# Kernel tuning notes

Measured on AMD Instinct MI355X. Metric: run time of the kernel, lower is better.

The kernel has to match this reference:

```python
import jax, jax.numpy as jnp
import numpy as np

T = 2048        # num tokens
HID = 2048      # hidden_size
HQ = 16         # num_heads
HKV = 8         # num_kv_heads
D = 128         # head_dim
P = 2           # power retention exponent
THETA = 10000.0 # rope base
SCALE = D ** -0.5


def setup_inputs() -> dict:
    key = jax.random.key(0)
    ks = jax.random.split(key, 8)
    s = 0.02
    return {
        "positions": jnp.arange(T, dtype=jnp.int64) if jax.config.jax_enable_x64 else jnp.arange(T, dtype=jnp.int32),
        "hidden_states": jax.random.normal(ks[0], (T, HID), jnp.float32),
        "Wq": jax.random.normal(ks[1], (HID, HQ * D), jnp.float32) * s,
        "bq": jnp.zeros((HQ * D,), jnp.float32),
        "Wk": jax.random.normal(ks[2], (HID, HKV * D), jnp.float32) * s,
        "bk": jnp.zeros((HKV * D,), jnp.float32),
        "Wv": jax.random.normal(ks[3], (HID, HKV * D), jnp.float32) * s,
        "bv": jnp.zeros((HKV * D,), jnp.float32),
        "Wg": jax.random.normal(ks[4], (HID, HKV), jnp.float32) * s,
        "bg": jnp.zeros((HKV,), jnp.float32),
        "Wo": jax.random.normal(ks[5], (HQ * D, HID), jnp.float32) * s,
        "bo": jnp.zeros((HID,), jnp.float32),
    }


def _rope_neox(x, pos):
    # x: [T, H, D], pos: [T]; rotate-half (neox) style, rotary_dim == head_dim
    half = D // 2
    inv_freq = 1.0 / (THETA ** (jnp.arange(0, D, 2, dtype=jnp.float32) / D))  # [D/2]
    freqs = pos.astype(jnp.float32)[:, None] * inv_freq                        # [T, D/2]
    cos = jnp.cos(freqs)[:, None, :]
    sin = jnp.sin(freqs)[:, None, :]
    x1, x2 = x[..., :half], x[..., half:]
    return jnp.concatenate([x1 * cos - x2 * sin, x2 * cos + x1 * sin], axis=-1)


def reference(positions, hidden_states, Wq, bq, Wk, bk, Wv, bv, Wg, bg, Wo, bo):
    # QKVG projections
    q = (hidden_states @ Wq + bq).reshape(T, HQ, D)
    k = (hidden_states @ Wk + bk).reshape(T, HKV, D)
    v = (hidden_states @ Wv + bv).reshape(T, HKV, D)
    g = hidden_states @ Wg + bg            # [T, HKV], one gate scalar per kv head

    # RoPE on q/k, logsigmoid gate in fp32
    q = _rope_neox(q, positions)
    k = _rope_neox(k, positions)
    g = jax.nn.log_sigmoid(g.astype(jnp.float32))   # [T, HKV], <= 0
    G = jnp.cumsum(g, axis=0)                       # [T, HKV] cumulative log-decay

    # GQA: expand kv heads to query heads
    rep = HQ // HKV
    k = jnp.repeat(k, rep, axis=1)   # [T, HQ, D]
    v = jnp.repeat(v, rep, axis=1)
    G = jnp.repeat(G, rep, axis=1)   # [T, HQ]

    # Power retention (quadratic attention form, seq_len <= switch_over_seq_len):
    # W_ij = (scale * q_i . k_j)^p * exp(G_i - G_j), causal j <= i
    S = jnp.einsum('thd,shd->hts', q, k) * SCALE      # [H, T, T]
    S = S ** P
    Gh = G.T                                          # [H, T]
    mask = jnp.tril(jnp.ones((T, T), dtype=bool))
    diff = jnp.where(mask[None], Gh[:, :, None] - Gh[:, None, :], -jnp.inf)
    W = S * jnp.exp(diff)                             # decay<=1 inside mask, 0 outside

    out = jnp.einsum('hts,shd->thd', W, v)            # [T, H, D]
    out = out.reshape(T, HQ * D) @ Wo + bo            # o_proj
    return out
```

## Files before the change

kernel.cpp:

```cpp
#include <hip/hip_runtime.h>
#include <hip/hip_bf16.h>
#include <math.h>

#define T_SEQ 2048
#define HID 2048
#define HQ 16
#define HKV 8
#define D_HEAD 128
#define HALF 64
#define SCALE_F 0.08838834764831845f
#define PROJW 4096

typedef __attribute__((ext_vector_type(8))) short bf16x8;
typedef __attribute__((ext_vector_type(4))) float f32x4;

static __device__ __forceinline__ short f2bf(float x) {
  unsigned u = __builtin_bit_cast(unsigned, x);
  unsigned r = (u + 0x7FFF + ((u >> 16) & 1)) >> 16;
  return (short)r;
}
static __device__ __forceinline__ float bf2f(unsigned short u) {
  unsigned v = ((unsigned)u) << 16;
  return __builtin_bit_cast(float, v);
}

#define GLDS(gsrc, ldst) \
  __builtin_amdgcn_global_load_lds((const __attribute__((address_space(1))) void*)(gsrc), \
                                   (__attribute__((address_space(3))) void*)(ldst), 16, 0, 0)

__global__ __launch_bounds__(256)
void cvt_bf16(const float* __restrict__ in, short* __restrict__ out, int n4)
{
  int i = blockIdx.x * blockDim.x + threadIdx.x;
  if (i >= n4) return;
  float4 v = reinterpret_cast<const float4*>(in)[i];
  short4 o;
  o.x = f2bf(v.x); o.y = f2bf(v.y); o.z = f2bf(v.z); o.w = f2bf(v.w);
  reinterpret_cast<short4*>(out)[i] = o;
}

__global__ __launch_bounds__(256)
void transpose_all(const float* __restrict__ Wq, const float* __restrict__ Wk,
                   const float* __restrict__ Wv, const float* __restrict__ Wo,
                   short* __restrict__ BTall, short* __restrict__ WoT)
{
  const int bx = blockIdx.x;
  const int k0 = blockIdx.y * 32;
  const float* src; short* dst; int Nsrc, n0;
  if (bx < 64)       { src = Wq; Nsrc = 2048; dst = BTall;                       n0 = bx * 32; }
  else if (bx < 96)  { src = Wk; Nsrc = 1024; dst = BTall + (size_t)2048 * 2048; n0 = (bx - 64) * 32; }
  else if (bx < 128) { src = Wv; Nsrc = 1024; dst = BTall + (size_t)3072 * 2048; n0 = (bx - 96) * 32; }
  else               { src = Wo; Nsrc = 2048; dst = WoT;                         n0 = (bx - 128) * 32; }

  __shared__ float tile[32][33];
  const int r = threadIdx.x >> 5, c = threadIdx.x & 31;
  #pragma unroll
  for (int i = 0; i < 4; ++i)
    tile[r + i * 8][c] = src[(size_t)(k0 + r + i * 8) * Nsrc + n0 + c];
  __syncthreads();
  const int n = threadIdx.x >> 3, k4 = (threadIdx.x & 7) * 4;
  short4 o;
  o.x = f2bf(tile[k4 + 0][n]); o.y = f2bf(tile[k4 + 1][n]);
  o.z = f2bf(tile[k4 + 2][n]); o.w = f2bf(tile[k4 + 3][n]);
  *reinterpret_cast<short4*>(&dst[(size_t)(n0 + n) * 2048 + k0 + k4]) = o;
}

__global__ __launch_bounds__(256)
void pack_bias(const float* __restrict__ bq, const float* __restrict__ bk,
               const float* __restrict__ bv, float* __restrict__ bcat)
{
  const int i = blockIdx.x * 256 + threadIdx.x;
  bcat[i] = (i < 2048) ? bq[i] : ((i < 3072) ? bk[i - 2048] : bv[i - 3072]);
}

template <bool OBF>
__global__ __launch_bounds__(256)
void gemm_bf16(const short* __restrict__ A, const short* __restrict__ BT,
               const float* __restrict__ bias, void* __restrict__ Cout,
               int N, int K)
{
  __shared__ short As[4][128 * 32];
  __shared__ short Bs[4][128 * 32];
  const int tid = threadIdx.x;
  const int wave = tid >> 6, lane = tid & 63;
  const int bm0 = blockIdx.y * 128, bn0 = blockIdx.x * 128;
  const int wm = (wave >> 1) * 64, wn = (wave & 1) * 64;

  const int srow = wave * 32 + (lane >> 2);
  const int scol = (lane & 3) * 8;
  const short* Abase = A + (size_t)(bm0 + srow) * K + scol;
  const short* Bbase = BT + (size_t)(bn0 + srow) * K + scol;

  f32x4 acc[4][4] = {};
  const int nk = K >> 5;

#define STAGE(buf, kk)                                                        \
  do {                                                                        \
    GLDS(Abase + ((kk) << 5), &As[buf][(wave * 32) * 32]);                    \
    GLDS(Abase + ((kk) << 5) + (size_t)16 * K, &As[buf][(wave * 32 + 16) * 32]); \
    GLDS(Bbase + ((kk) << 5), &Bs[buf][(wave * 32) * 32]);                    \
    GLDS(Bbase + ((kk) << 5) + (size_t)16 * K, &Bs[buf][(wave * 32 + 16) * 32]); \
  } while (0)

  STAGE(0, 0);
  STAGE(1, 1);
  asm volatile("s_waitcnt vmcnt(4)" ::: "memory");
  asm volatile("s_barrier" ::: "memory");
  __builtin_amdgcn_sched_barrier(0);

  const int kof = (lane >> 4) * 8;
  const int rA = wm + (lane & 15);
  const int rB = wn + (lane & 15);

  for (int t = 0; t < nk; ++t) {
    const int cur = t & 3;
    if (t + 2 < nk) STAGE((t + 2) & 3, t + 2);

    bf16x8 af[4], bfr[4];
    #pragma unroll
    for (int i = 0; i < 4; ++i) {
      af[i]  = *reinterpret_cast<const bf16x8*>(&As[cur][(rA + i * 16) * 32 + kof]);
      bfr[i] = *reinterpret_cast<const bf16x8*>(&Bs[cur][(rB + i * 16) * 32 + kof]);
    }
    #pragma unroll
    for (int i = 0; i < 4; ++i)
      #pragma unroll
      for (int j = 0; j < 4; ++j)
        acc[i][j] = __builtin_amdgcn_mfma_f32_16x16x32_bf16(af[i], bfr[j], acc[i][j], 0, 0, 0);

    if (t + 1 < nk) {
      if (t + 2 < nk) asm volatile("s_waitcnt vmcnt(4)" ::: "memory");
      else            asm volatile("s_waitcnt vmcnt(0)" ::: "memory");
      asm volatile("s_barrier" ::: "memory");
      __builtin_amdgcn_sched_barrier(0);
    }
  }

  const int crow = wm + (lane >> 4) * 4;
  const int ccol = wn + (lane & 15);
  #pragma unroll
  for (int j = 0; j < 4; ++j) {
    const int col = bn0 + ccol + j * 16;
    const float b = bias[col];
    #pragma unroll
    for (int i = 0; i < 4; ++i)
      #pragma unroll
      for (int r = 0; r < 4; ++r) {
        const int row = bm0 + crow + i * 16 + r;
        const float v = acc[i][j][r] + b;
        if constexpr (OBF)
          ((short*)Cout)[(size_t)row * N + col] = f2bf(v);
        else
          ((float*)Cout)[(size_t)row * N + col] = v;
      }
  }
#undef STAGE
}

__global__ __launch_bounds__(256)
void gproj_kernel(const float* __restrict__ hs, const float* __restrict__ Wg,
                  const float* __restrict__ bg, float* __restrict__ gT)
{
  const int t = blockIdx.x, tid = threadIdx.x;
  __shared__ float red[256][9];
  float a[8] = {0.f, 0.f, 0.f, 0.f, 0.f, 0.f, 0.f, 0.f};
  for (int cc = tid; cc < HID; cc += 256) {
    const float hv = hs[(size_t)t * HID + cc];
    const float4 w0 = *reinterpret_cast<const float4*>(Wg + (size_t)cc * 8);
    const float4 w1 = *reinterpret_cast<const float4*>(Wg + (size_t)cc * 8 + 4);
    a[0] = fmaf(hv, w0.x, a[0]); a[1] = fmaf(hv, w0.y, a[1]);
    a[2] = fmaf(hv, w0.z, a[2]); a[3] = fmaf(hv, w0.w, a[3]);
    a[4] = fmaf(hv, w1.x, a[4]); a[5] = fmaf(hv, w1.y, a[5]);
    a[6] = fmaf(hv, w1.z, a[6]); a[7] = fmaf(hv, w1.w, a[7]);
  }
  #pragma unroll
  for (int j = 0; j < 8; ++j) red[tid][j] = a[j];
  __syncthreads();
  for (int s = 128; s >= 1; s >>= 1) {
    if (tid < s) {
      #pragma unroll
      for (int j = 0; j < 8; ++j) red[tid][j] += red[tid + s][j];
    }
    __syncthreads();
  }
  if (tid < 8) {
    const float x = red[0][tid] + bg[tid];
    const float nx = -x;
    const float sp = (nx > 20.f) ? nx : log1pf(expf(nx));
    gT[(size_t)tid * T_SEQ + t] = -sp;
  }
}

__global__ __launch_bounds__(512)
void gscan_kernel(const float* __restrict__ gT, float* __restrict__ Gct)
{
  const int h = blockIdx.x;
  const int tid = threadIdx.x;
  const int wid = tid >> 6, lane = tid & 63;
  __shared__ float wsum[8];

  const float4 v = reinterpret_cast<const float4*>(gT + (size_t)h * T_SEQ)[tid];
  const float p0 = v.x, p1 = p0 + v.y, p2 = p1 + v.z, p3 = p2 + v.w;

  float sc = p3;
  #pragma unroll
  for (int off = 1; off < 64; off <<= 1) {
    const float o = __shfl_up(sc, off, 64);
    if (lane >= off) sc += o;
  }
  if (lane == 63) wsum[wid] = sc;
  __syncthreads();
  float wof = 0.f;
  #pragma unroll
  for (int w = 0; w < 8; ++w) wof += (w < wid) ? wsum[w] : 0.f;

  const float excl = wof + sc - p3;
  reinterpret_cast<float4*>(Gct + (size_t)h * T_SEQ)[tid] =
      make_float4(excl + p0, excl + p1, excl + p2, excl + p3);
}

__global__ __launch_bounds__(192)
void rope_kernel(short* __restrict__ proj)
{
  const int t = blockIdx.x;
  __shared__ float cs[64], sn[64];
  if (threadIdx.x < 64) {
    const int i = threadIdx.x;
    const float f = (float)t * powf(10000.0f, -(float)i / 64.0f);
    cs[i] = cosf(f); sn[i] = sinf(f);
  }
  __syncthreads();
  const int u = threadIdx.x;
  const int hh = u >> 3, ch = u & 7;
  short* base = proj + (size_t)t * PROJW +
                ((hh < HQ) ? hh * D_HEAD : 2048 + (hh - HQ) * D_HEAD);
  bf16x8 x1 = *reinterpret_cast<bf16x8*>(base + ch * 8);
  bf16x8 x2 = *reinterpret_cast<bf16x8*>(base + HALF + ch * 8);
  #pragma unroll
  for (int j = 0; j < 8; ++j) {
    const float a = bf2f((unsigned short)x1[j]);
    const float b = bf2f((unsigned short)x2[j]);
    const float cc = cs[ch * 8 + j], ss = sn[ch * 8 + j];
    x1[j] = f2bf(a * cc - b * ss);
    x2[j] = f2bf(b * cc + a * ss);
  }
  *reinterpret_cast<bf16x8*>(base + ch * 8) = x1;
  *reinterpret_cast<bf16x8*>(base + HALF + ch * 8) = x2;
}

__global__ __launch_bounds__(256)
void vtrans_kernel(const unsigned short* __restrict__ proj, unsigned short* __restrict__ vt)
{
  __shared__ unsigned short tile[32][33];
  const int tt = blockIdx.x * 32, dd = blockIdx.y * 32, hk = blockIdx.z;
  const int c = threadIdx.x & 31, r0 = (threadIdx.x >> 5) * 4;
  #pragma unroll
  for (int i = 0; i < 4; ++i)
    tile[r0 + i][c] = proj[(size_t)(tt + r0 + i) * PROJW + 3072 + hk * 128 + dd + c];
  __syncthreads();
  #pragma unroll
  for (int i = 0; i < 4; ++i)
    vt[(size_t)(hk * 128 + dd + r0 + i) * T_SEQ + tt + c] = tile[c][r0 + i];
}

__global__ __launch_bounds__(256, 1)
void attn_mfma(const short* __restrict__ proj, const short* __restrict__ vt,
               const float* __restrict__ Gct, short* __restrict__ outb)
{
  __shared__ __align__(16) char smem[86528];
  const int hk = blockIdx.x;
  const int tb = blockIdx.y * 64;
  const int tid = threadIdx.x;
  const int wid = tid >> 6, lane = tid & 63;
  const int c = lane & 15, g = lane >> 4;
  const int h = 2 * hk + (wid >> 1);
  const int tw = tb + (wid & 1) * 32;
  const float* Gh = Gct + (size_t)hk * T_SEQ;

  const float glim = Gh[tb] + 90.0f;
  int lo = 0, hi = tb;
  while (lo < hi) {
    const int mid = (lo + hi) >> 1;
    if (Gh[mid] > glim) lo = mid + 1; else hi = mid;
  }
  const int sfirst = lo & ~63;
  const int nst = ((tb - sfirst) >> 6) + 1;

  bf16x8 qf[2][4];
  #pragma unroll
  for (int tt = 0; tt < 2; ++tt)
    #pragma unroll
    for (int kb = 0; kb < 4; ++kb)
      qf[tt][kb] = *reinterpret_cast<const bf16x8*>(
          proj + (size_t)(tw + 16 * tt + c) * PROJW + h * D_HEAD + kb * 32 + g * 8);
  const float gt0 = Gh[tw + c];
  const float gt1 = Gh[tw + 16 + c];
  const float gtw = Gh[tw];
  const int twmax = tw + 31;

  f32x4 accv[2][8] = {};

#define ASTG(buf, s64)                                                                   \
  do {                                                                                   \
    _Pragma("unroll")                                                                    \
    for (int i2 = 0; i2 < 4; ++i2) {                                                     \
      const int cid = tid + 256 * i2;                                                    \
      const int kr = cid >> 4, kc = cid & 15;                                            \
      GLDS(proj + (size_t)((s64) + kr) * PROJW + 2048 + hk * 128 + ((kc ^ (kr & 7)) * 8),\
           smem + (buf) * 16384 + cid * 16);                                             \
      const int vr = cid >> 3, vc = cid & 7;                                             \
      GLDS(vt + (size_t)(hk * 128 + vr) * T_SEQ + (s64) + ((vc ^ (vr & 7)) * 8),         \
           smem + 32768 + (buf) * 16384 + cid * 16);                                     \
    }                                                                                    \
    if (tid < 64) ((float*)(smem + 86016))[(buf) * 64 + tid] = Gh[(s64) + tid];          \
  } while (0)

  ASTG(0, sfirst);
  __syncthreads();

  for (int i = 0; i < nst; ++i) {
    const int cur = i & 1;
    if (i + 1 < nst) ASTG(cur ^ 1, sfirst + (i + 1) * 64);
    const int sbase64 = sfirst + i * 64;
    const float* Gss = (const float*)(smem + 86016) + cur * 64;
    char* Pmy = smem + 65536 + wid * 5120;

    #pragma unroll
    for (int st = 0; st < 2; ++st) {
      const int s0 = sbase64 + st * 32;
      if (s0 > twmax) continue;
      if (gtw - Gss[st * 32 + 31] < -90.0f) continue;

      bf16x8 kf[2][4];
      #pragma unroll
      for (int sg = 0; sg < 2; ++sg)
        #pragma unroll
        for (int kb = 0; kb < 4; ++kb) {
          const int row = st * 32 + 16 * sg + c;
          const int byt = (row * 256 + kb * 64 + g * 16) ^ ((c & 7) << 4);
          kf[sg][kb] = *reinterpret_cast<const bf16x8*>(smem + cur * 16384 + byt);
        }
      f32x4 sa[2][2] = {};
      #pragma unroll
      for (int kb = 0; kb < 4; ++kb)
        #pragma unroll
        for (int sg = 0; sg < 2; ++sg)
          #pragma unroll
          for (int tt = 0; tt < 2; ++tt)
            sa[sg][tt] = __builtin_amdgcn_mfma_f32_16x16x32_bf16(
                kf[sg][kb], qf[tt][kb], sa[sg][tt], 0, 0, 0);

      #pragma unroll
      for (int sg = 0; sg < 2; ++sg) {
        const float4 gs = *reinterpret_cast<const float4*>(&Gss[st * 32 + sg * 16 + g * 4]);
        const float gsv[4] = {gs.x, gs.y, gs.z, gs.w};
        #pragma unroll
        for (int tt = 0; tt < 2; ++tt) {
          const int tg = tw + 16 * tt + c;
          const float gt = tt ? gt1 : gt0;
          const int sg0 = s0 + sg * 16 + g * 4;
          float w[4];
          #pragma unroll
          for (int r = 0; r < 4; ++r) {
            const float dv = sa[sg][tt][r] * SCALE_F;
            const float ww = dv * dv * __expf(gt - gsv[r]);
            w[r] = (sg0 + r <= tg) ? ww : 0.0f;
          }
          uint2 pv;
          pv.x = ((unsigned)(unsigned short)f2bf(w[1]) << 16) | (unsigned short)f2bf(w[0]);
          pv.y = ((unsigned)(unsigned short)f2bf(w[3]) << 16) | (unsigned short)f2bf(w[2]);
          *reinterpret_cast<uint2*>(Pmy + st * 2560 + (c + 16 * tt) * 80 + 8 * g + 32 * sg) = pv;
        }
      }
      asm volatile("s_waitcnt lgkmcnt(0)" ::: "memory");
      __builtin_amdgcn_sched_barrier(0);

      bf16x8 pf[2];
      #pragma unroll
      for (int tt = 0; tt < 2; ++tt)
        pf[tt] = *reinterpret_cast<const bf16x8*>(Pmy + st * 2560 + (c + 16 * tt) * 80 + g * 16);

      #pragma unroll
      for (int db = 0; db < 8; ++db) {
        const int row = 16 * db + c;
        const int byt = (row * 128 + st * 64 + g * 16) ^ ((c & 7) << 4);
        const bf16x8 vf = *reinterpret_cast<const bf16x8*>(smem + 32768 + cur * 16384 + byt);
        #pragma unroll
        for (int tt = 0; tt < 2; ++tt)
          accv[tt][db] = __builtin_amdgcn_mfma_f32_16x16x32_bf16(pf[tt], vf, accv[tt][db], 0, 0, 0);
      }
    }
    __syncthreads();
  }

  char* Wme = smem + wid * 8704;
  #pragma unroll
  for (int tt = 0; tt < 2; ++tt)
    #pragma unroll
    for (int db = 0; db < 8; ++db)
      #pragma unroll
      for (int r = 0; r < 4; ++r)
        *reinterpret_cast<short*>(Wme + (16 * tt + 4 * g + r) * 272 + (16 * db + c) * 2)
            = f2bf(accv[tt][db][r]);
  asm volatile("s_waitcnt lgkmcnt(0)" ::: "memory");
  __builtin_amdgcn_sched_barrier(0);
  #pragma unroll
  for (int e = 0; e < 8; ++e) {
    const int idx = e * 64 + lane;
    const int tr = idx >> 4, d0 = (idx & 15) * 8;
    const bf16x8 vv = *reinterpret_cast<const bf16x8*>(Wme + tr * 272 + d0 * 2);
    *reinterpret_cast<bf16x8*>(outb + ((size_t)(tw + tr) * HQ + h) * D_HEAD + d0) = vv;
  }
#undef ASTG
}

extern "C" void kernel_launch(void* const* d_in, const int* in_sizes, int n_in,
                              void* d_out, int out_size, void* d_ws, size_t ws_size,
                              hipStream_t stream)
{
  const float* hs = (const float*)d_in[1];
  const float* Wq = (const float*)d_in[2];
  const float* bq = (const float*)d_in[3];
  const float* Wk = (const float*)d_in[4];
  const float* bk = (const float*)d_in[5];
  const float* Wv = (const float*)d_in[6];
  const float* bv = (const float*)d_in[7];
  const float* Wg = (const float*)d_in[8];
  const float* bg = (const float*)d_in[9];
  const float* Wo = (const float*)d_in[10];
  const float* bo = (const float*)d_in[11];
  float* outp = (float*)d_out;

  short* proj  = (short*)d_ws;
  short* vtb   = proj + (size_t)T_SEQ * PROJW;
  float* gT    = (float*)(vtb + (size_t)HKV * D_HEAD * T_SEQ);
  float* Gct   = gT + 16384;
  float* bcat  = Gct + 16384;
  short* hsb   = (short*)(bcat + 4096);
  short* BTall = hsb + (size_t)2048 * 2048;
  short* WoT   = BTall + (size_t)4096 * 2048;
  short* attnout = hsb;

  cvt_bf16<<<4096, 256, 0, stream>>>(hs, hsb, 1048576);
  transpose_all<<<dim3(192, 64), 256, 0, stream>>>(Wq, Wk, Wv, Wo, BTall, WoT);
  pack_bias<<<16, 256, 0, stream>>>(bq, bk, bv, bcat);

  gproj_kernel<<<2048, 256, 0, stream>>>(hs, Wg, bg, gT);
  gscan_kernel<<<8, 512, 0, stream>>>(gT, Gct);

  gemm_bf16<true><<<dim3(32, 16), 256, 0, stream>>>(
      hsb, BTall, bcat, proj, PROJW, 2048);

  rope_kernel<<<2048, 192, 0, stream>>>(proj);
  vtrans_kernel<<<dim3(64, 4, 8), 256, 0, stream>>>((const unsigned short*)proj,
                                                    (unsigned short*)vtb);

  attn_mfma<<<dim3(8, 32), 256, 0, stream>>>(proj, vtb, Gct, attnout);

  gemm_bf16<false><<<dim3(16, 16), 256, 0, stream>>>(
      attnout, WoT, bo, outp, 2048, 2048);
}
```

Before: 152.2 us.

## Replace bf16 GEMM with wider 128x256 tile, swizzled LDS, 512-thread kernel

```diff
diff --git a/kernel.cpp b/kernel.cpp
--- a/kernel.cpp
+++ b/kernel.cpp
@@ -74,70 +74,103 @@
 }
 
 template <bool OBF>
-__global__ __launch_bounds__(256)
-void gemm_bf16(const short* __restrict__ A, const short* __restrict__ BT,
+__global__ __launch_bounds__(512, 2)
+void gemm_wide(const short* __restrict__ A, const short* __restrict__ BT,
                const float* __restrict__ bias, void* __restrict__ Cout,
                int N, int K)
 {
-  __shared__ short As[4][128 * 32];
-  __shared__ short Bs[4][128 * 32];
+  __shared__ __align__(16) char Alds[2][16384];
+  __shared__ __align__(16) char Blds[2][32768];
   const int tid = threadIdx.x;
-  const int wave = tid >> 6, lane = tid & 63;
-  const int bm0 = blockIdx.y * 128, bn0 = blockIdx.x * 128;
-  const int wm = (wave >> 1) * 64, wn = (wave & 1) * 64;
-
-  const int srow = wave * 32 + (lane >> 2);
-  const int scol = (lane & 3) * 8;
-  const short* Abase = A + (size_t)(bm0 + srow) * K + scol;
-  const short* Bbase = BT + (size_t)(bn0 + srow) * K + scol;
+  const int wid = tid >> 6, lane = tid & 63;
+  const int bm0 = blockIdx.y * 128, bn0 = blockIdx.x * 256;
+  const int wr = wid >> 2, wc = wid & 3;
+  const int c = lane & 15, g = lane >> 4;
+  const int xv = (c & 7) << 4;
 
   f32x4 acc[4][4] = {};
-  const int nk = K >> 5;
-
-#define STAGE(buf, kk)                                                        \
-  do {                                                                        \
-    GLDS(Abase + ((kk) << 5), &As[buf][(wave * 32) * 32]);                    \
-    GLDS(Abase + ((kk) << 5) + (size_t)16 * K, &As[buf][(wave * 32 + 16) * 32]); \
-    GLDS(Bbase + ((kk) << 5), &Bs[buf][(wave * 32) * 32]);                    \
-    GLDS(Bbase + ((kk) << 5) + (size_t)16 * K, &Bs[buf][(wave * 32 + 16) * 32]); \
+  const int nk = K >> 6;
+
+#define STG_A(buf, kt)                                                          \
+  do {                                                                          \
+    const int ci0 = wid * 64 + lane;                                            \
+    const int r0 = ci0 >> 3, c0 = ((ci0 & 7) ^ (r0 & 7)) * 8;                   \
+    GLDS(A + (size_t)(bm0 + r0) * K + (kt) * 64 + c0,                           \
+         &Alds[buf][(wid * 64) * 16]);                                          \
+    const int ci1 = ci0 + 512;                                                  \
+    const int r1 = ci1 >> 3, c1 = ((ci1 & 7) ^ (r1 & 7)) * 8;                   \
+    GLDS(A + (size_t)(bm0 + r1) * K + (kt) * 64 + c1,                           \
+         &Alds[buf][(wid * 64 + 512) * 16]);                                    \
   } while (0)
-
-  STAGE(0, 0);
-  STAGE(1, 1);
-  asm volatile("s_waitcnt vmcnt(4)" ::: "memory");
+#define STG_B(buf, kt, jj)                                                      \
+  do {                                                                          \
+    const int ci0 = wid * 64 + lane + (jj) * 512;                               \
+    const int r0 = ci0 >> 3, c0 = ((ci0 & 7) ^ (r0 & 7)) * 8;                   \
+    GLDS(BT + (size_t)(bn0 + r0) * K + (kt) * 64 + c0,                          \
+         &Blds[buf][(wid * 64 + (jj) * 512) * 16]);                             \
+    const int ci1 = ci0 + 512;                                                  \
+    const int r1 = ci1 >> 3, c1 = ((ci1 & 7) ^ (r1 & 7)) * 8;                   \
+    GLDS(BT + (size_t)(bn0 + r1) * K + (kt) * 64 + c1,                          \
+         &Blds[buf][(wid * 64 + (jj) * 512 + 512) * 16]);                       \
+  } while (0)
+
+  STG_A(0, 0); STG_B(0, 0, 0); STG_B(0, 0, 2);
+  asm volatile("s_waitcnt vmcnt(0)" ::: "memory");
   asm volatile("s_barrier" ::: "memory");
   __builtin_amdgcn_sched_barrier(0);
 
-  const int kof = (lane >> 4) * 8;
-  const int rA = wm + (lane & 15);
-  const int rB = wn + (lane & 15);
-
   for (int t = 0; t < nk; ++t) {
-    const int cur = t & 3;
-    if (t + 2 < nk) STAGE((t + 2) & 3, t + 2);
-
-    bf16x8 af[4], bfr[4];
-    #pragma unroll
-    for (int i = 0; i < 4; ++i) {
-      af[i]  = *reinterpret_cast<const bf16x8*>(&As[cur][(rA + i * 16) * 32 + kof]);
-      bfr[i] = *reinterpret_cast<const bf16x8*>(&Bs[cur][(rB + i * 16) * 32 + kof]);
+    const int p = t & 1, q = p ^ 1;
+    const bool pre = (t + 1 < nk);
+
+    if (pre) { STG_A(q, t + 1); STG_B(q, t + 1, 0); }
+    {
+      bf16x8 a[4], b[4];
+      #pragma unroll
+      for (int m = 0; m < 4; ++m)
+        a[m] = *reinterpret_cast<const bf16x8*>(
+            &Alds[p][(((wr * 64 + m * 16 + c) * 128) + g * 16) ^ xv]);
+      #pragma unroll
+      for (int n = 0; n < 4; ++n)
+        b[n] = *reinterpret_cast<const bf16x8*>(
+            &Blds[p][(((wc * 64 + n * 16 + c) * 128) + g * 16) ^ xv]);
+      __builtin_amdgcn_s_setprio(1);
+      #pragma unroll
+      for (int m = 0; m < 4; ++m)
+        #pragma unroll
+        for (int n = 0; n < 4; ++n)
+          acc[m][n] = __builtin_amdgcn_mfma_f32_16x16x32_bf16(a[m], b[n], acc[m][n], 0, 0, 0);
+      __builtin_amdgcn_s_setprio(0);
     }
-    #pragma unroll
-    for (int i = 0; i < 4; ++i)
-      #pragma unroll
-      for (int j = 0; j < 4; ++j)
-        acc[i][j] = __builtin_amdgcn_mfma_f32_16x16x32_bf16(af[i], bfr[j], acc[i][j], 0, 0, 0);
-
-    if (t + 1 < nk) {
-      if (t + 2 < nk) asm volatile("s_waitcnt vmcnt(4)" ::: "memory");
-      else            asm volatile("s_waitcnt vmcnt(0)" ::: "memory");
-      asm volatile("s_barrier" ::: "memory");
-      __builtin_amdgcn_sched_barrier(0);
+    asm volatile("s_barrier" ::: "memory");
+    __builtin_amdgcn_sched_barrier(0);
+
+    if (pre) { STG_B(q, t + 1, 2); }
+    {
+      bf16x8 a[4], b[4];
+      #pragma unroll
+      for (int m = 0; m < 4; ++m)
+        a[m] = *reinterpret_cast<const bf16x8*>(
+            &Alds[p][(((wr * 64 + m * 16 + c) * 128) + 64 + g * 16) ^ xv]);
+      #pragma unroll
+      for (int n = 0; n < 4; ++n)
+        b[n] = *reinterpret_cast<const bf16x8*>(
+            &Blds[p][(((wc * 64 + n * 16 + c) * 128) + 64 + g * 16) ^ xv]);
+      __builtin_amdgcn_s_setprio(1);
+      #pragma unroll
+      for (int m = 0; m < 4; ++m)
+        #pragma unroll
+        for (int n = 0; n < 4; ++n)
+          acc[m][n] = __builtin_amdgcn_mfma_f32_16x16x32_bf16(a[m], b[n], acc[m][n], 0, 0, 0);
+      __builtin_amdgcn_s_setprio(0);
     }
-  }
-
-  const int crow = wm + (lane >> 4) * 4;
-  const int ccol = wn + (lane & 15);
+    if (pre) asm volatile("s_waitcnt vmcnt(0)" ::: "memory");
+    asm volatile("s_barrier" ::: "memory");
+    __builtin_amdgcn_sched_barrier(0);
+  }
+
+  const int crow = wr * 64 + g * 4;
+  const int ccol = wc * 64 + c;
   #pragma unroll
   for (int j = 0; j < 4; ++j) {
     const int col = bn0 + ccol + j * 16;
@@ -154,7 +187,8 @@
           ((float*)Cout)[(size_t)row * N + col] = v;
       }
   }
-#undef STAGE
+#undef STG_A
+#undef STG_B
 }
 
 __global__ __launch_bounds__(256)
@@ -448,7 +482,7 @@
   gproj_kernel<<<2048, 256, 0, stream>>>(hs, Wg, bg, gT);
   gscan_kernel<<<8, 512, 0, stream>>>(gT, Gct);
 
-  gemm_bf16<true><<<dim3(32, 16), 256, 0, stream>>>(
+  gemm_wide<true><<<dim3(16, 16), 512, 0, stream>>>(
       hsb, BTall, bcat, proj, PROJW, 2048);
 
   rope_kernel<<<2048, 192, 0, stream>>>(proj);
@@ -457,6 +491,6 @@
 
   attn_mfma<<<dim3(8, 32), 256, 0, stream>>>(proj, vtb, Gct, attnout);
 
-  gemm_bf16<false><<<dim3(16, 16), 256, 0, stream>>>(
+  gemm_wide<false><<<dim3(8, 16), 512, 0, stream>>>(
       attnout, WoT, bo, outp, 2048, 2048);
 }
```

Measured after the change: 173.7 us. +14.1%, slower.

## Replace bf16 GEMMs with 8-wave 256x128 swizzled GEMM and split-K output projection

Applied to the files above, without the earlier changes.

```diff
diff --git a/kernel.cpp b/kernel.cpp
--- a/kernel.cpp
+++ b/kernel.cpp
@@ -73,88 +73,177 @@
   bcat[i] = (i < 2048) ? bq[i] : ((i < 3072) ? bk[i - 2048] : bv[i - 3072]);
 }
 
+__global__ __launch_bounds__(256)
+void add_f32(float* __restrict__ out, const float* __restrict__ part, int n4)
+{
+  int i = blockIdx.x * blockDim.x + threadIdx.x;
+  if (i >= n4) return;
+  float4 a = reinterpret_cast<float4*>(out)[i];
+  const float4 b = reinterpret_cast<const float4*>(part)[i];
+  a.x += b.x; a.y += b.y; a.z += b.z; a.w += b.w;
+  reinterpret_cast<float4*>(out)[i] = a;
+}
+
 template <bool OBF>
-__global__ __launch_bounds__(256)
-void gemm_bf16(const short* __restrict__ A, const short* __restrict__ BT,
-               const float* __restrict__ bias, void* __restrict__ Cout,
-               int N, int K)
-{
-  __shared__ short As[4][128 * 32];
-  __shared__ short Bs[4][128 * 32];
-  const int tid = threadIdx.x;
-  const int wave = tid >> 6, lane = tid & 63;
-  const int bm0 = blockIdx.y * 128, bn0 = blockIdx.x * 128;
-  const int wm = (wave >> 1) * 64, wn = (wave & 1) * 64;
-
-  const int srow = wave * 32 + (lane >> 2);
-  const int scol = (lane & 3) * 8;
-  const short* Abase = A + (size_t)(bm0 + srow) * K + scol;
-  const short* Bbase = BT + (size_t)(bn0 + srow) * K + scol;
+__global__ __launch_bounds__(512, 1)
+void gemm8p(const short* __restrict__ A, const short* __restrict__ BT,
+            const float* __restrict__ bias, void* __restrict__ Cout0,
+            void* __restrict__ Cout1, int N, int Kst, int klen)
+{
+  __shared__ __align__(16) short Al[3][256 * 64];
+  __shared__ __align__(16) short Bl[3][128 * 64];
+  const int tid = threadIdx.x, wid = tid >> 6, lane = tid & 63;
+  const int z = blockIdx.z;
+  const int koff = z * klen;
+  const int nwg = gridDim.x * gridDim.y;
+  const int orig = blockIdx.y * gridDim.x + blockIdx.x;
+  const int swz = (orig & 7) * (nwg >> 3) + (orig >> 3);
+  const int bx = swz % gridDim.x, by = swz / gridDim.x;
+  const int bm0 = by * 256, bn0 = bx * 128;
+  const int wr = wid >> 1, wc = wid & 1;
+  const int c = lane & 15, g = lane >> 4;
+  const int xc = (c & 7) << 4;
+  const int nk = klen >> 6;
 
   f32x4 acc[4][4] = {};
-  const int nk = K >> 5;
-
-#define STAGE(buf, kk)                                                        \
-  do {                                                                        \
-    GLDS(Abase + ((kk) << 5), &As[buf][(wave * 32) * 32]);                    \
-    GLDS(Abase + ((kk) << 5) + (size_t)16 * K, &As[buf][(wave * 32 + 16) * 32]); \
-    GLDS(Bbase + ((kk) << 5), &Bs[buf][(wave * 32) * 32]);                    \
-    GLDS(Bbase + ((kk) << 5) + (size_t)16 * K, &Bs[buf][(wave * 32 + 16) * 32]); \
+
+#define STGA(p, kt, j) do {                                                   \
+    const int cid = (j) * 512 + wid * 64 + lane;                              \
+    const int rr = cid >> 3;                                                  \
+    const int gx = (cid & 7) ^ (rr & 7);                                      \
+    GLDS(A + (size_t)(bm0 + rr) * Kst + koff + (kt) * 64 + gx * 8,            \
+         &Al[p][((j) * 512 + wid * 64) * 8]);                                 \
   } while (0)
-
-  STAGE(0, 0);
-  STAGE(1, 1);
-  asm volatile("s_waitcnt vmcnt(4)" ::: "memory");
-  asm volatile("s_barrier" ::: "memory");
+#define STGB(p, kt, j) do {                                                   \
+    const int cid = (j) * 512 + wid * 64 + lane;                              \
+    const int rr = cid >> 3;                                                  \
+    const int gx = (cid & 7) ^ (rr & 7);                                      \
+    GLDS(BT + (size_t)(bn0 + rr) * Kst + koff + (kt) * 64 + gx * 8,           \
+         &Bl[p][((j) * 512 + wid * 64) * 8]);                                 \
+  } while (0)
+
+#define RDA(p, mh, mm, ks)                                                    \
+  (*reinterpret_cast<const bf16x8*>((const char*)&Al[p][0] +                  \
+      (size_t)(wr * 64 + (mh) * 32 + (mm) * 16 + c) * 128 +                   \
+      (((ks) * 64 + g * 16) ^ xc)))
+#define RDB(p, nh, nn, ks)                                                    \
+  (*reinterpret_cast<const bf16x8*>((const char*)&Bl[p][0] +                  \
+      (size_t)(wc * 64 + (nh) * 32 + (nn) * 16 + c) * 128 +                   \
+      (((ks) * 64 + g * 16) ^ xc)))
+
+  STGA(0, 0, 0); STGA(0, 0, 1); STGA(0, 0, 2); STGA(0, 0, 3);
+  STGB(0, 0, 0); STGB(0, 0, 1);
+  if (nk > 1) {
+    STGA(1, 1, 0); STGA(1, 1, 1); STGA(1, 1, 2); STGA(1, 1, 3);
+    STGB(1, 1, 0); STGB(1, 1, 1);
+    asm volatile("s_waitcnt vmcnt(6)" ::: "memory");
+  } else {
+    asm volatile("s_waitcnt vmcnt(0)" ::: "memory");
+  }
+  __builtin_amdgcn_s_barrier();
   __builtin_amdgcn_sched_barrier(0);
 
-  const int kof = (lane >> 4) * 8;
-  const int rA = wm + (lane & 15);
-  const int rB = wn + (lane & 15);
+  bf16x8 aR[2][2], b0R[2][2], b1R[2][2];
 
   for (int t = 0; t < nk; ++t) {
-    const int cur = t & 3;
-    if (t + 2 < nk) STAGE((t + 2) & 3, t + 2);
-
-    bf16x8 af[4], bfr[4];
-    #pragma unroll
-    for (int i = 0; i < 4; ++i) {
-      af[i]  = *reinterpret_cast<const bf16x8*>(&As[cur][(rA + i * 16) * 32 + kof]);
-      bfr[i] = *reinterpret_cast<const bf16x8*>(&Bs[cur][(rB + i * 16) * 32 + kof]);
-    }
-    #pragma unroll
-    for (int i = 0; i < 4; ++i)
-      #pragma unroll
-      for (int j = 0; j < 4; ++j)
-        acc[i][j] = __builtin_amdgcn_mfma_f32_16x16x32_bf16(af[i], bfr[j], acc[i][j], 0, 0, 0);
-
-    if (t + 1 < nk) {
-      if (t + 2 < nk) asm volatile("s_waitcnt vmcnt(4)" ::: "memory");
-      else            asm volatile("s_waitcnt vmcnt(0)" ::: "memory");
-      asm volatile("s_barrier" ::: "memory");
-      __builtin_amdgcn_sched_barrier(0);
-    }
-  }
-
-  const int crow = wm + (lane >> 4) * 4;
-  const int ccol = wn + (lane & 15);
-  #pragma unroll
-  for (int j = 0; j < 4; ++j) {
-    const int col = bn0 + ccol + j * 16;
-    const float b = bias[col];
-    #pragma unroll
-    for (int i = 0; i < 4; ++i)
-      #pragma unroll
-      for (int r = 0; r < 4; ++r) {
-        const int row = bm0 + crow + i * 16 + r;
-        const float v = acc[i][j][r] + b;
+    const int p = t % 3;
+    const int s2 = (t + 2) % 3;
+    const bool pre = (t + 2 < nk);
+
+    #pragma unroll
+    for (int mm = 0; mm < 2; ++mm) { aR[mm][0] = RDA(p, 0, mm, 0); aR[mm][1] = RDA(p, 0, mm, 1); }
+    #pragma unroll
+    for (int nn = 0; nn < 2; ++nn) { b0R[nn][0] = RDB(p, 0, nn, 0); b0R[nn][1] = RDB(p, 0, nn, 1); }
+    if (pre) { STGA(s2, t + 2, 0); STGA(s2, t + 2, 1); }
+    __builtin_amdgcn_s_barrier();
+    asm volatile("s_waitcnt lgkmcnt(0)" ::: "memory");
+    __builtin_amdgcn_sched_barrier(0);
+    __builtin_amdgcn_s_setprio(1);
+    #pragma unroll
+    for (int ks = 0; ks < 2; ++ks)
+      #pragma unroll
+      for (int mm = 0; mm < 2; ++mm)
+        #pragma unroll
+        for (int nn = 0; nn < 2; ++nn)
+          acc[mm][nn] = __builtin_amdgcn_mfma_f32_16x16x32_bf16(aR[mm][ks], b0R[nn][ks], acc[mm][nn], 0, 0, 0);
+    __builtin_amdgcn_s_setprio(0);
+    __builtin_amdgcn_s_barrier();
+
+    #pragma unroll
+    for (int nn = 0; nn < 2; ++nn) { b1R[nn][0] = RDB(p, 1, nn, 0); b1R[nn][1] = RDB(p, 1, nn, 1); }
+    if (pre) { STGA(s2, t + 2, 2); STGA(s2, t + 2, 3); }
+    __builtin_amdgcn_s_barrier();
+    asm volatile("s_waitcnt lgkmcnt(0)" ::: "memory");
+    __builtin_amdgcn_sched_barrier(0);
+    __builtin_amdgcn_s_setprio(1);
+    #pragma unroll
+    for (int ks = 0; ks < 2; ++ks)
+      #pragma unroll
+      for (int mm = 0; mm < 2; ++mm)
+        #pragma unroll
+        for (int nn = 0; nn < 2; ++nn)
+          acc[mm][2 + nn] = __builtin_amdgcn_mfma_f32_16x16x32_bf16(aR[mm][ks], b1R[nn][ks], acc[mm][2 + nn], 0, 0, 0);
+    __builtin_amdgcn_s_setprio(0);
+    __builtin_amdgcn_s_barrier();
+
+    #pragma unroll
+    for (int mm = 0; mm < 2; ++mm) { aR[mm][0] = RDA(p, 1, mm, 0); aR[mm][1] = RDA(p, 1, mm, 1); }
+    if (pre) STGB(s2, t + 2, 0);
+    __builtin_amdgcn_s_barrier();
+    asm volatile("s_waitcnt lgkmcnt(0)" ::: "memory");
+    __builtin_amdgcn_sched_barrier(0);
+    __builtin_amdgcn_s_setprio(1);
+    #pragma unroll
+    for (int ks = 0; ks < 2; ++ks)
+      #pragma unroll
+      for (int mm = 0; mm < 2; ++mm)
+        #pragma unroll
+        for (int nn = 0; nn < 2; ++nn)
+          acc[2 + mm][2 + nn] = __builtin_amdgcn_mfma_f32_16x16x32_bf16(aR[mm][ks], b1R[nn][ks], acc[2 + mm][2 + nn], 0, 0, 0);
+    __builtin_amdgcn_s_setprio(0);
+    __builtin_amdgcn_s_barrier();
+
+    if (pre) STGB(s2, t + 2, 1);
+    __builtin_amdgcn_s_barrier();
+    __builtin_amdgcn_sched_barrier(0);
+    __builtin_amdgcn_s_setprio(1);
+    #pragma unroll
+    for (int ks = 0; ks < 2; ++ks)
+      #pragma unroll
+      for (int mm = 0; mm < 2; ++mm)
+        #pragma unroll
+        for (int nn = 0; nn < 2; ++nn)
+          acc[2 + mm][nn] = __builtin_amdgcn_mfma_f32_16x16x32_bf16(aR[mm][ks], b0R[nn][ks], acc[2 + mm][nn], 0, 0, 0);
+    __builtin_amdgcn_s_setprio(0);
+    if (pre)                asm volatile("s_waitcnt vmcnt(6)" ::: "memory");
+    else if (t + 1 < nk)    asm volatile("s_waitcnt vmcnt(0)" ::: "memory");
+    __builtin_amdgcn_s_barrier();
+    __builtin_amdgcn_sched_barrier(0);
+  }
+
+  void* Cout = (z == 0) ? Cout0 : Cout1;
+  const int crow = bm0 + wr * 64 + g * 4;
+  const int ccol = bn0 + wc * 64 + c;
+  #pragma unroll
+  for (int nf = 0; nf < 4; ++nf) {
+    const int col = ccol + nf * 16;
+    const float b = (z == 0) ? bias[col] : 0.f;
+    #pragma unroll
+    for (int mf = 0; mf < 4; ++mf)
+      #pragma unroll
+      for (int rr = 0; rr < 4; ++rr) {
+        const int row = crow + mf * 16 + rr;
+        const float v = acc[mf][nf][rr] + b;
         if constexpr (OBF)
           ((short*)Cout)[(size_t)row * N + col] = f2bf(v);
         else
           ((float*)Cout)[(size_t)row * N + col] = v;
       }
   }
-#undef STAGE
+#undef STGA
+#undef STGB
+#undef RDA
+#undef RDB
 }
 
 __global__ __launch_bounds__(256)
@@ -440,6 +529,7 @@
   short* BTall = hsb + (size_t)2048 * 2048;
   short* WoT   = BTall + (size_t)4096 * 2048;
   short* attnout = hsb;
+  float* opart   = (float*)BTall;
 
   cvt_bf16<<<4096, 256, 0, stream>>>(hs, hsb, 1048576);
   transpose_all<<<dim3(192, 64), 256, 0, stream>>>(Wq, Wk, Wv, Wo, BTall, WoT);
@@ -448,8 +538,8 @@
   gproj_kernel<<<2048, 256, 0, stream>>>(hs, Wg, bg, gT);
   gscan_kernel<<<8, 512, 0, stream>>>(gT, Gct);
 
-  gemm_bf16<true><<<dim3(32, 16), 256, 0, stream>>>(
-      hsb, BTall, bcat, proj, PROJW, 2048);
+  gemm8p<true><<<dim3(32, 8, 1), 512, 0, stream>>>(
+      hsb, BTall, bcat, proj, proj, PROJW, 2048, 2048);
 
   rope_kernel<<<2048, 192, 0, stream>>>(proj);
   vtrans_kernel<<<dim3(64, 4, 8), 256, 0, stream>>>((const unsigned short*)proj,
@@ -457,6 +547,7 @@
 
   attn_mfma<<<dim3(8, 32), 256, 0, stream>>>(proj, vtb, Gct, attnout);
 
-  gemm_bf16<false><<<dim3(16, 16), 256, 0, stream>>>(
-      attnout, WoT, bo, outp, 2048, 2048);
-}
+  gemm8p<false><<<dim3(16, 8, 2), 512, 0, stream>>>(
+      attnout, WoT, bo, outp, opart, 2048, 2048, 1024);
+  add_f32<<<4096, 256, 0, stream>>>(outp, opart, 1048576);
+}
```

New measurement: 145.7 us. -4.3%, faster.
